# Kernel optimization log

Hardware: AMD Instinct MI355X
Metric: run time of the kernel (lower is better)

## Reference

```python
import jax, jax.numpy as jnp
import numpy as np

N_NODES = 100000
N_EDGES = 1600000
HIDDEN = 128
LEAKY_SLOPE = 0.01  # torch F.leaky_relu default


def setup_inputs() -> dict:
    key = jax.random.key(0)
    k1, k2, k3, k4 = jax.random.split(key, 4)
    x = jax.random.normal(k1, (N_NODES, HIDDEN), dtype=jnp.float32)
    edge_index = jax.random.randint(k2, (2, N_EDGES), 0, N_NODES, dtype=jnp.int64)
    # nn.Linear(hidden, 1, bias=False) weights, stored as [hidden] vectors
    w_i = jax.random.normal(k3, (HIDDEN,), dtype=jnp.float32) * (1.0 / np.sqrt(HIDDEN))
    w_j = jax.random.normal(k4, (HIDDEN,), dtype=jnp.float32) * (1.0 / np.sqrt(HIDDEN))
    return {"x": x, "edge_index": edge_index, "w_i": w_i, "w_j": w_j}


def _segment_softmax(e, seg, num_segments):
    # numerically stable softmax over variable-length groups keyed by seg
    seg_max = jax.ops.segment_max(e, seg, num_segments=num_segments)
    seg_max = jnp.where(jnp.isfinite(seg_max), seg_max, 0.0)  # empty segments
    e_exp = jnp.exp(e - seg_max[seg])
    denom = jax.ops.segment_sum(e_exp, seg, num_segments=num_segments)
    return e_exp / denom[seg]


def reference(x, edge_index, w_i, w_j):
    n = x.shape[0]
    idx_j = edge_index[0]  # edge_index_j (softmax groups)
    idx_i = edge_index[1]  # edge_index_i (aggregation destinations)
    # per-node attention logits, gathered per edge
    ei_all = x @ w_i  # [N]
    ej_all = x @ w_j  # [N]
    e = ei_all[idx_i] + ej_all[idx_j]  # [E]
    e = jnp.where(e > 0, e, LEAKY_SLOPE * e)  # leaky_relu
    alpha = _segment_softmax(e.astype(jnp.float32), idx_j, n)  # [E]
    # spmm(edge_index[[1,0]], alpha, N, N, x): out[idx_i] += alpha * x[idx_j]
    msgs = alpha[:, None] * x[idx_j]  # [E, hidden]
    out = jax.ops.segment_sum(msgs, idx_i, num_segments=n)
    return jax.nn.relu(out)
```

## Files before the change

kernel.cpp:

```cpp
#include <hip/hip_runtime.h>

#define N_HID 128
#define LEAKY 0.01f
#define EPB   2048
#define SCB   1024
#define TABV(g) (tab[g] + bs1[(g) >> 10])

__device__ inline ushort f2bf_rne(float f) {
    unsigned u = __float_as_uint(f);
    u += 0x7fffu + ((u >> 16) & 1u);
    return (ushort)(u >> 16);
}

__device__ inline int load_idx(const void* eidx, long long pos, int is64) {
    if (is64) return (int)((const long long*)eidx)[pos];
    return ((const int*)eidx)[pos];
}

__global__ void detect_dtype_k(const void* __restrict__ eidx, long long n_i64,
                               int* __restrict__ flag) {
    __shared__ int nonzero_hi;
    if (threadIdx.x == 0) nonzero_hi = 0;
    __syncthreads();
    const long long* p = (const long long*)eidx;
    long long samples = n_i64 < 4096 ? n_i64 : 4096;
    int bad = 0;
    for (long long k = threadIdx.x; k < samples; k += blockDim.x) {
        if ((p[k] >> 32) != 0) bad = 1;
    }
    if (bad) atomicOr(&nonzero_hi, 1);
    __syncthreads();
    if (threadIdx.x == 0) *flag = nonzero_hi ? 0 : 1;
}

__global__ __launch_bounds__(256) void node_logits_k(
        const float* __restrict__ x, const float* __restrict__ w_i,
        const float* __restrict__ w_j, float* __restrict__ ei_all,
        float* __restrict__ ej_all, ushort* __restrict__ xb, int n) {
    int wave = (int)((blockIdx.x * (long long)blockDim.x + threadIdx.x) >> 6);
    int lane = threadIdx.x & 63;
    if (wave >= n) return;
    const float2* xr = (const float2*)(x + (long long)wave * N_HID);
    float2 v  = xr[lane];
    float2 wi = ((const float2*)w_i)[lane];
    float2 wj = ((const float2*)w_j)[lane];
    if (xb) {
        unsigned packed = (unsigned)f2bf_rne(v.x) | ((unsigned)f2bf_rne(v.y) << 16);
        ((unsigned*)(xb + (long long)wave * N_HID))[lane] = packed;
    }
    float si = v.x * wi.x + v.y * wi.y;
    float sj = v.x * wj.x + v.y * wj.y;
    #pragma unroll
    for (int off = 32; off >= 1; off >>= 1) {
        si += __shfl_xor(si, off);
        sj += __shfl_xor(sj, off);
    }
    if (lane == 0) {
        ei_all[wave] = si;
        ej_all[wave] = sj;
    }
}

__global__ __launch_bounds__(256) void hist_k(
        const void* __restrict__ eidx, const int* __restrict__ flag,
        unsigned* __restrict__ tabI, unsigned* __restrict__ tabJ,
        long long E, int nblkA, int NB) {
    __shared__ unsigned hi[512], hj[512];
    for (int b = threadIdx.x; b < NB; b += 256) { hi[b] = 0; hj[b] = 0; }
    __syncthreads();
    int is64 = *flag;
    long long k0 = (long long)blockIdx.x * EPB;
    #pragma unroll 4
    for (int m = 0; m < EPB / 256; ++m) {
        long long k = k0 + m * 256 + threadIdx.x;
        if (k < E) {
            int j = load_idx(eidx, k, is64);
            int i = load_idx(eidx, E + k, is64);
            atomicAdd(&hi[i >> 8], 1u);
            atomicAdd(&hj[j >> 8], 1u);
        }
    }
    __syncthreads();
    for (int b = threadIdx.x; b < NB; b += 256) {
        tabI[(size_t)b * nblkA + blockIdx.x] = hi[b];
        tabJ[(size_t)b * nblkA + blockIdx.x] = hj[b];
    }
}

__global__ __launch_bounds__(SCB) void scanT1_k(unsigned* __restrict__ a,
                                                unsigned* __restrict__ bs, int nt) {
    __shared__ unsigned tmp[SCB];
    int gid = blockIdx.x * SCB + threadIdx.x;
    unsigned v = (gid < nt) ? a[gid] : 0;
    tmp[threadIdx.x] = v;
    __syncthreads();
    for (int off = 1; off < SCB; off <<= 1) {
        unsigned t = (threadIdx.x >= off) ? tmp[threadIdx.x - off] : 0;
        __syncthreads();
        tmp[threadIdx.x] += t;
        __syncthreads();
    }
    if (gid < nt) a[gid] = tmp[threadIdx.x] - v;
    if (threadIdx.x == SCB - 1) bs[blockIdx.x] = tmp[threadIdx.x];
}

__global__ __launch_bounds__(SCB) void scanT2_k(unsigned* __restrict__ bs, int nb) {
    __shared__ unsigned tmp[SCB];
    unsigned v = (threadIdx.x < nb) ? bs[threadIdx.x] : 0;
    tmp[threadIdx.x] = v;
    __syncthreads();
    for (int off = 1; off < SCB; off <<= 1) {
        unsigned t = (threadIdx.x >= off) ? tmp[threadIdx.x - off] : 0;
        __syncthreads();
        tmp[threadIdx.x] += t;
        __syncthreads();
    }
    if (threadIdx.x < nb) bs[threadIdx.x] = tmp[threadIdx.x] - v;
}

__global__ __launch_bounds__(256) void scatter2_k(
        const void* __restrict__ eidx, const int* __restrict__ flag,
        const unsigned* __restrict__ tab, const unsigned* __restrict__ bs1,
        unsigned* __restrict__ srecI, unsigned* __restrict__ srecJ,
        long long E, int nblkA, int NB, int NT) {
    __shared__ unsigned ci[512], cj[512];
    unsigned Eu = (unsigned)E;
    for (int b = threadIdx.x; b < NB; b += 256) {
        size_t gI = (size_t)b * nblkA + blockIdx.x;
        size_t gJ = (size_t)NT + gI;
        ci[b] = TABV(gI);
        cj[b] = TABV(gJ) - Eu;
    }
    __syncthreads();
    int is64 = *flag;
    long long k0 = (long long)blockIdx.x * EPB;
    #pragma unroll 4
    for (int m = 0; m < EPB / 256; ++m) {
        long long k = k0 + m * 256 + threadIdx.x;
        if (k < E) {
            int j = load_idx(eidx, k, is64);
            int i = load_idx(eidx, E + k, is64);
            unsigned pI = atomicAdd(&ci[i >> 8], 1u);
            srecI[pI] = ((unsigned)(i & 255) << 17) | (unsigned)j;
            unsigned pJ = atomicAdd(&cj[j >> 8], 1u);
            srecJ[pJ] = ((unsigned)(j & 255) << 17) | (unsigned)i;
        }
    }
}

__global__ __launch_bounds__(512) void finalizeJ_k(
        const unsigned* __restrict__ srecJ, const unsigned* __restrict__ tab,
        const unsigned* __restrict__ bs1, const float* __restrict__ ei_all,
        const float* __restrict__ ej_all, float2* __restrict__ ejd,
        int n, long long E, int nblkA, int NB, int NT) {
    int b = blockIdx.x;
    int tid = threadIdx.x;
    unsigned Eu = (unsigned)E;
    size_t gJ0 = (size_t)NT + (size_t)b * nblkA;
    int base = (int)(TABV(gJ0) - Eu);
    int end  = (b + 1 < NB) ? (int)(TABV(gJ0 + nblkA) - Eu) : (int)E;

    __shared__ float ejl[256];
    __shared__ float dsum[256];
    int g = b * 256 + tid;
    if (tid < 256) {
        ejl[tid]  = (g < n) ? ej_all[g] : 0.f;
        dsum[tid] = 0.f;
    }
    __syncthreads();

    for (int t = base + tid; t < end; t += 512) {
        unsigned r = srecJ[t];
        int jl = (int)(r >> 17);
        int i  = (int)(r & 0x1FFFFu);
        float e = ei_all[i] + ejl[jl];
        e = e > 0.f ? e : LEAKY * e;
        atomicAdd(&dsum[jl], __expf(e));
    }
    __syncthreads();
    if (tid < 256 && g < n) {
        float2 r2;
        r2.x = ejl[tid];
        r2.y = dsum[tid];
        ejd[g] = r2;
    }
}

__global__ __launch_bounds__(512) void finalizeI_k(
        const unsigned* __restrict__ srecI, const unsigned* __restrict__ tab,
        const unsigned* __restrict__ bs1, const float* __restrict__ ei_all,
        const float2* __restrict__ ejd, int* __restrict__ start,
        unsigned* __restrict__ pje, int n, long long E, int nblkA, int NB,
        int NT) {
    int b = blockIdx.x;
    int tid = threadIdx.x;
    size_t gI0 = (size_t)b * nblkA;
    int base = (int)TABV(gI0);
    int end  = (b + 1 < NB) ? (int)TABV(gI0 + nblkA) : (int)E;

    __shared__ int cnt[256];
    __shared__ int off[256];
    __shared__ float eil[256];
    int g = b * 256 + tid;
    if (tid < 256) {
        cnt[tid] = 0;
        eil[tid] = (g < n) ? ei_all[g] : 0.f;
    }
    __syncthreads();

    for (int t = base + tid; t < end; t += 512)
        atomicAdd(&cnt[srecI[t] >> 17], 1);
    __syncthreads();

    int v = 0;
    if (tid < 256) { v = cnt[tid]; off[tid] = v; }
    __syncthreads();
    for (int s = 1; s < 256; s <<= 1) {
        int t2 = 0;
        if (tid < 256 && tid >= s) t2 = off[tid - s];
        __syncthreads();
        if (tid < 256) off[tid] += t2;
        __syncthreads();
    }
    if (tid < 256) {
        int excl = off[tid] - v;
        if (g < n) start[g] = base + excl;
        cnt[tid] = excl;
    }
    if (b == NB - 1 && tid == 0) start[n] = (int)E;
    __syncthreads();

    for (int t = base + tid; t < end; t += 512) {
        unsigned r = srecI[t];
        int il = (int)(r >> 17);
        int j  = (int)(r & 0x1FFFFu);
        float2 ed = ejd[j];
        float e = eil[il] + ed.x;
        e = e > 0.f ? e : LEAKY * e;
        float alpha = __expf(e) / ed.y;
        unsigned aq = __float2uint_rn(alpha * 32768.f);
        if (aq > 32767u) aq = 32767u;
        int slot = base + atomicAdd(&cnt[il], 1);
        pje[slot] = ((unsigned)j << 15) | aq;
    }
}

__global__ __launch_bounds__(256) void gather_bf16_k(
        const int* __restrict__ start, const unsigned* __restrict__ pje,
        const ushort* __restrict__ xb, float* __restrict__ out, int n) {
    int wave = (int)((blockIdx.x * (long long)blockDim.x + threadIdx.x) >> 6);
    int lane = threadIdx.x & 63;
    if (wave >= n) return;
    int s = start[wave];
    int e_end = start[wave + 1];
    int sub = lane >> 4;
    int col = lane & 15;

    float a0 = 0.f, a1 = 0.f, a2 = 0.f, a3 = 0.f;
    float a4 = 0.f, a5 = 0.f, a6 = 0.f, a7 = 0.f;
    for (int e = s; e < e_end; e += 8) {
        int ee0 = e + sub;
        int ee1 = e + 4 + sub;
        unsigned cur0 = (ee0 < e_end) ? pje[ee0] : 0u;
        unsigned cur1 = (ee1 < e_end) ? pje[ee1] : 0u;
        float af0 = (float)(cur0 & 0x7FFFu) * (1.f / 32768.f);
        float af1 = (float)(cur1 & 0x7FFFu) * (1.f / 32768.f);
        uint4 u0 = ((const uint4*)(xb + (size_t)(cur0 >> 15) * N_HID))[col];
        uint4 u1 = ((const uint4*)(xb + (size_t)(cur1 >> 15) * N_HID))[col];
        a0 += af0 * __uint_as_float(u0.x << 16);
        a1 += af0 * __uint_as_float(u0.x & 0xffff0000u);
        a2 += af0 * __uint_as_float(u0.y << 16);
        a3 += af0 * __uint_as_float(u0.y & 0xffff0000u);
        a4 += af0 * __uint_as_float(u0.z << 16);
        a5 += af0 * __uint_as_float(u0.z & 0xffff0000u);
        a6 += af0 * __uint_as_float(u0.w << 16);
        a7 += af0 * __uint_as_float(u0.w & 0xffff0000u);
        a0 += af1 * __uint_as_float(u1.x << 16);
        a1 += af1 * __uint_as_float(u1.x & 0xffff0000u);
        a2 += af1 * __uint_as_float(u1.y << 16);
        a3 += af1 * __uint_as_float(u1.y & 0xffff0000u);
        a4 += af1 * __uint_as_float(u1.z << 16);
        a5 += af1 * __uint_as_float(u1.z & 0xffff0000u);
        a6 += af1 * __uint_as_float(u1.w << 16);
        a7 += af1 * __uint_as_float(u1.w & 0xffff0000u);
    }
    a0 += __shfl_xor(a0, 16); a1 += __shfl_xor(a1, 16);
    a2 += __shfl_xor(a2, 16); a3 += __shfl_xor(a3, 16);
    a4 += __shfl_xor(a4, 16); a5 += __shfl_xor(a5, 16);
    a6 += __shfl_xor(a6, 16); a7 += __shfl_xor(a7, 16);
    a0 += __shfl_xor(a0, 32); a1 += __shfl_xor(a1, 32);
    a2 += __shfl_xor(a2, 32); a3 += __shfl_xor(a3, 32);
    a4 += __shfl_xor(a4, 32); a5 += __shfl_xor(a5, 32);
    a6 += __shfl_xor(a6, 32); a7 += __shfl_xor(a7, 32);

    float4* orow = (float4*)(out + (size_t)wave * N_HID);
    if (sub == 0) {
        float4 r;
        r.x = fmaxf(a0, 0.f); r.y = fmaxf(a1, 0.f);
        r.z = fmaxf(a2, 0.f); r.w = fmaxf(a3, 0.f);
        orow[col * 2] = r;
    } else if (sub == 1) {
        float4 r;
        r.x = fmaxf(a4, 0.f); r.y = fmaxf(a5, 0.f);
        r.z = fmaxf(a6, 0.f); r.w = fmaxf(a7, 0.f);
        orow[col * 2 + 1] = r;
    }
}

__global__ __launch_bounds__(256) void gather_f32_k(
        const int* __restrict__ start, const unsigned* __restrict__ pje,
        const float* __restrict__ x, float* __restrict__ out, int n) {
    int wave = (int)((blockIdx.x * (long long)blockDim.x + threadIdx.x) >> 6);
    int lane = threadIdx.x & 63;
    if (wave >= n) return;
    int s = start[wave];
    int e_end = start[wave + 1];
    float ax = 0.f, ay = 0.f;
    unsigned ja = 0;
    if (s < e_end) ja = pje[s];
    for (int e = s; e < e_end; ++e) {
        unsigned cur = ja;
        if (e + 1 < e_end) ja = pje[e + 1];
        float a = (float)(cur & 0x7FFFu) * (1.f / 32768.f);
        float2 v = ((const float2*)(x + (long long)(cur >> 15) * N_HID))[lane];
        ax += a * v.x;
        ay += a * v.y;
    }
    float2 r;
    r.x = fmaxf(ax, 0.f);
    r.y = fmaxf(ay, 0.f);
    ((float2*)(out + (long long)wave * N_HID))[lane] = r;
}

extern "C" void kernel_launch(void* const* d_in, const int* in_sizes, int n_in,
                              void* d_out, int out_size, void* d_ws,
                              size_t ws_size, hipStream_t stream) {
    const float* x   = (const float*)d_in[0];
    const void*  eix = d_in[1];
    const float* w_i = (const float*)d_in[2];
    const float* w_j = (const float*)d_in[3];
    float* out = (float*)d_out;

    int n = in_sizes[0] / N_HID;
    long long E = in_sizes[1] / 2;

    int nblkA = (int)((E + EPB - 1) / EPB);
    int NB    = (n + 255) / 256;
    int NT    = NB * nblkA;
    int NT2   = 2 * NT;
    int nb1   = (NT2 + SCB - 1) / SCB;

    char* p = (char*)d_ws;
    float* ei_all = (float*)p;               p += (size_t)n * 4;
    float* ej_all = (float*)p;               p += (size_t)n * 4;
    float2* ejd   = (float2*)p;              p += (size_t)n * 8;
    int*   start  = (int*)p;                 p += ((size_t)(n + 1) * 4 + 15) & ~15ull;
    unsigned* tab = (unsigned*)p;            p += ((size_t)NT2 * 4 + 15) & ~15ull;
    unsigned* tabI = tab;
    unsigned* tabJ = tab + NT;
    unsigned* bs1 = (unsigned*)p;            p += (size_t)SCB * 4;
    int*   flag   = (int*)p;                 p += 16;
    unsigned* srecI = (unsigned*)p;          p += (size_t)E * 4;
    unsigned* pje   = (unsigned*)p;          p += (size_t)E * 4;
    unsigned* srecJ = pje;
    ushort* xb    = (ushort*)p;              p += (size_t)n * N_HID * 2;
    int wsBig = ((size_t)(p - (char*)d_ws) <= ws_size);
    if (!wsBig) xb = nullptr;

    detect_dtype_k<<<1, 256, 0, stream>>>(eix, E * 2, flag);

    long long t1 = (long long)n * 64;
    node_logits_k<<<(unsigned)((t1 + 255) / 256), 256, 0, stream>>>(
        x, w_i, w_j, ei_all, ej_all, xb, n);

    hist_k<<<nblkA, 256, 0, stream>>>(eix, flag, tabI, tabJ, E, nblkA, NB);

    scanT1_k<<<nb1, SCB, 0, stream>>>(tab, bs1, NT2);
    scanT2_k<<<1, SCB, 0, stream>>>(bs1, nb1);

    scatter2_k<<<nblkA, 256, 0, stream>>>(eix, flag, tab, bs1, srecI, srecJ,
                                          E, nblkA, NB, NT);

    finalizeJ_k<<<NB, 512, 0, stream>>>(srecJ, tab, bs1, ei_all, ej_all, ejd,
                                        n, E, nblkA, NB, NT);

    finalizeI_k<<<NB, 512, 0, stream>>>(srecI, tab, bs1, ei_all, ejd,
                                        start, pje, n, E, nblkA, NB, NT);

    long long t4 = (long long)n * 64;
    if (wsBig) {
        gather_bf16_k<<<(unsigned)((t4 + 255) / 256), 256, 0, stream>>>(
            start, pje, xb, out, n);
    } else {
        gather_f32_k<<<(unsigned)((t4 + 255) / 256), 256, 0, stream>>>(
            start, pje, x, out, n);
    }
}
```

Before: 201.9 us.

## Fuse logits and histogram kernels, inline dtype detection, prefetch edge records

Merges the node-logit kernel and the edge histogram kernel into one launch, splitting blocks by index between the two jobs so the independent work can run side by side. The separate dtype-detection kernel and its flag buffer are removed; each wave now samples 64 index words with a ballot. The gather loop also software-prefetches the next packed edge records. This cuts two launches and their serial dependencies, at the cost of a weaker dtype check that samples fewer values.

```diff
diff --git a/kernel.cpp b/kernel.cpp
--- a/kernel.cpp
+++ b/kernel.cpp
@@ -17,73 +17,64 @@
     return ((const int*)eidx)[pos];
 }
 
-__global__ void detect_dtype_k(const void* __restrict__ eidx, long long n_i64,
-                               int* __restrict__ flag) {
-    __shared__ int nonzero_hi;
-    if (threadIdx.x == 0) nonzero_hi = 0;
-    __syncthreads();
+__device__ inline int detect64(const void* eidx, int lane) {
     const long long* p = (const long long*)eidx;
-    long long samples = n_i64 < 4096 ? n_i64 : 4096;
-    int bad = 0;
-    for (long long k = threadIdx.x; k < samples; k += blockDim.x) {
-        if ((p[k] >> 32) != 0) bad = 1;
-    }
-    if (bad) atomicOr(&nonzero_hi, 1);
-    __syncthreads();
-    if (threadIdx.x == 0) *flag = nonzero_hi ? 0 : 1;
-}
-
-__global__ __launch_bounds__(256) void node_logits_k(
+    unsigned long long b = __ballot((p[lane] >> 32) != 0);
+    return b == 0ull;
+}
+
+__global__ __launch_bounds__(256) void logits_hist_k(
         const float* __restrict__ x, const float* __restrict__ w_i,
         const float* __restrict__ w_j, float* __restrict__ ei_all,
-        float* __restrict__ ej_all, ushort* __restrict__ xb, int n) {
-    int wave = (int)((blockIdx.x * (long long)blockDim.x + threadIdx.x) >> 6);
+        float* __restrict__ ej_all, ushort* __restrict__ xb,
+        const void* __restrict__ eidx, unsigned* __restrict__ tabI,
+        unsigned* __restrict__ tabJ, int n, long long E,
+        int nblkA, int NB) {
+    __shared__ unsigned hi[512], hj[512];
     int lane = threadIdx.x & 63;
-    if (wave >= n) return;
-    const float2* xr = (const float2*)(x + (long long)wave * N_HID);
-    float2 v  = xr[lane];
-    float2 wi = ((const float2*)w_i)[lane];
-    float2 wj = ((const float2*)w_j)[lane];
-    if (xb) {
-        unsigned packed = (unsigned)f2bf_rne(v.x) | ((unsigned)f2bf_rne(v.y) << 16);
-        ((unsigned*)(xb + (long long)wave * N_HID))[lane] = packed;
-    }
-    float si = v.x * wi.x + v.y * wi.y;
-    float sj = v.x * wj.x + v.y * wj.y;
-    #pragma unroll
-    for (int off = 32; off >= 1; off >>= 1) {
-        si += __shfl_xor(si, off);
-        sj += __shfl_xor(sj, off);
-    }
-    if (lane == 0) {
-        ei_all[wave] = si;
-        ej_all[wave] = sj;
-    }
-}
-
-__global__ __launch_bounds__(256) void hist_k(
-        const void* __restrict__ eidx, const int* __restrict__ flag,
-        unsigned* __restrict__ tabI, unsigned* __restrict__ tabJ,
-        long long E, int nblkA, int NB) {
-    __shared__ unsigned hi[512], hj[512];
-    for (int b = threadIdx.x; b < NB; b += 256) { hi[b] = 0; hj[b] = 0; }
-    __syncthreads();
-    int is64 = *flag;
-    long long k0 = (long long)blockIdx.x * EPB;
-    #pragma unroll 4
-    for (int m = 0; m < EPB / 256; ++m) {
-        long long k = k0 + m * 256 + threadIdx.x;
-        if (k < E) {
-            int j = load_idx(eidx, k, is64);
-            int i = load_idx(eidx, E + k, is64);
-            atomicAdd(&hi[i >> 8], 1u);
-            atomicAdd(&hj[j >> 8], 1u);
-        }
-    }
-    __syncthreads();
-    for (int b = threadIdx.x; b < NB; b += 256) {
-        tabI[(size_t)b * nblkA + blockIdx.x] = hi[b];
-        tabJ[(size_t)b * nblkA + blockIdx.x] = hj[b];
+    if (blockIdx.x < (unsigned)nblkA) {
+        for (int b = threadIdx.x; b < NB; b += 256) { hi[b] = 0; hj[b] = 0; }
+        __syncthreads();
+        int is64 = detect64(eidx, lane);
+        long long k0 = (long long)blockIdx.x * EPB;
+        #pragma unroll 4
+        for (int m = 0; m < EPB / 256; ++m) {
+            long long k = k0 + m * 256 + threadIdx.x;
+            if (k < E) {
+                int j = load_idx(eidx, k, is64);
+                int i = load_idx(eidx, E + k, is64);
+                atomicAdd(&hi[i >> 8], 1u);
+                atomicAdd(&hj[j >> 8], 1u);
+            }
+        }
+        __syncthreads();
+        for (int b = threadIdx.x; b < NB; b += 256) {
+            tabI[(size_t)b * nblkA + blockIdx.x] = hi[b];
+            tabJ[(size_t)b * nblkA + blockIdx.x] = hj[b];
+        }
+    } else {
+        int blk = blockIdx.x - nblkA;
+        int wave = blk * 4 + (int)(threadIdx.x >> 6);
+        if (wave >= n) return;
+        const float2* xr = (const float2*)(x + (long long)wave * N_HID);
+        float2 v  = xr[lane];
+        float2 wi = ((const float2*)w_i)[lane];
+        float2 wj = ((const float2*)w_j)[lane];
+        if (xb) {
+            unsigned pk = (unsigned)f2bf_rne(v.x) | ((unsigned)f2bf_rne(v.y) << 16);
+            ((unsigned*)(xb + (long long)wave * N_HID))[lane] = pk;
+        }
+        float si = v.x * wi.x + v.y * wi.y;
+        float sj = v.x * wj.x + v.y * wj.y;
+        #pragma unroll
+        for (int off = 32; off >= 1; off >>= 1) {
+            si += __shfl_xor(si, off);
+            sj += __shfl_xor(sj, off);
+        }
+        if (lane == 0) {
+            ei_all[wave] = si;
+            ej_all[wave] = sj;
+        }
     }
 }
 
@@ -119,10 +110,9 @@
 }
 
 __global__ __launch_bounds__(256) void scatter2_k(
-        const void* __restrict__ eidx, const int* __restrict__ flag,
-        const unsigned* __restrict__ tab, const unsigned* __restrict__ bs1,
-        unsigned* __restrict__ srecI, unsigned* __restrict__ srecJ,
-        long long E, int nblkA, int NB, int NT) {
+        const void* __restrict__ eidx, const unsigned* __restrict__ tab,
+        const unsigned* __restrict__ bs1, unsigned* __restrict__ srecI,
+        unsigned* __restrict__ srecJ, long long E, int nblkA, int NB, int NT) {
     __shared__ unsigned ci[512], cj[512];
     unsigned Eu = (unsigned)E;
     for (int b = threadIdx.x; b < NB; b += 256) {
@@ -132,7 +122,7 @@
         cj[b] = TABV(gJ) - Eu;
     }
     __syncthreads();
-    int is64 = *flag;
+    int is64 = detect64(eidx, threadIdx.x & 63);
     long long k0 = (long long)blockIdx.x * EPB;
     #pragma unroll 4
     for (int m = 0; m < EPB / 256; ++m) {
@@ -258,11 +248,14 @@
 
     float a0 = 0.f, a1 = 0.f, a2 = 0.f, a3 = 0.f;
     float a4 = 0.f, a5 = 0.f, a6 = 0.f, a7 = 0.f;
+    int p0 = s + sub, p1 = s + 4 + sub;
+    unsigned nc0 = (p0 < e_end) ? pje[p0] : 0u;
+    unsigned nc1 = (p1 < e_end) ? pje[p1] : 0u;
     for (int e = s; e < e_end; e += 8) {
-        int ee0 = e + sub;
-        int ee1 = e + 4 + sub;
-        unsigned cur0 = (ee0 < e_end) ? pje[ee0] : 0u;
-        unsigned cur1 = (ee1 < e_end) ? pje[ee1] : 0u;
+        unsigned cur0 = nc0, cur1 = nc1;
+        int q0 = e + 8 + sub, q1 = e + 12 + sub;
+        nc0 = (q0 < e_end) ? pje[q0] : 0u;
+        nc1 = (q1 < e_end) ? pje[q1] : 0u;
         float af0 = (float)(cur0 & 0x7FFFu) * (1.f / 32768.f);
         float af1 = (float)(cur1 & 0x7FFFu) * (1.f / 32768.f);
         uint4 u0 = ((const uint4*)(xb + (size_t)(cur0 >> 15) * N_HID))[col];
@@ -345,6 +338,7 @@
     long long E = in_sizes[1] / 2;
 
     int nblkA = (int)((E + EPB - 1) / EPB);
+    int nblkL = (n + 3) / 4;
     int NB    = (n + 255) / 256;
     int NT    = NB * nblkA;
     int NT2   = 2 * NT;
@@ -359,7 +353,6 @@
     unsigned* tabI = tab;
     unsigned* tabJ = tab + NT;
     unsigned* bs1 = (unsigned*)p;            p += (size_t)SCB * 4;
-    int*   flag   = (int*)p;                 p += 16;
     unsigned* srecI = (unsigned*)p;          p += (size_t)E * 4;
     unsigned* pje   = (unsigned*)p;          p += (size_t)E * 4;
     unsigned* srecJ = pje;
@@ -367,18 +360,13 @@
     int wsBig = ((size_t)(p - (char*)d_ws) <= ws_size);
     if (!wsBig) xb = nullptr;
 
-    detect_dtype_k<<<1, 256, 0, stream>>>(eix, E * 2, flag);
-
-    long long t1 = (long long)n * 64;
-    node_logits_k<<<(unsigned)((t1 + 255) / 256), 256, 0, stream>>>(
-        x, w_i, w_j, ei_all, ej_all, xb, n);
-
-    hist_k<<<nblkA, 256, 0, stream>>>(eix, flag, tabI, tabJ, E, nblkA, NB);
+    logits_hist_k<<<(unsigned)(nblkA + nblkL), 256, 0, stream>>>(
+        x, w_i, w_j, ei_all, ej_all, xb, eix, tabI, tabJ, n, E, nblkA, NB);
 
     scanT1_k<<<nb1, SCB, 0, stream>>>(tab, bs1, NT2);
     scanT2_k<<<1, SCB, 0, stream>>>(bs1, nb1);
 
-    scatter2_k<<<nblkA, 256, 0, stream>>>(eix, flag, tab, bs1, srecI, srecJ,
+    scatter2_k<<<nblkA, 256, 0, stream>>>(eix, tab, bs1, srecI, srecJ,
                                           E, nblkA, NB, NT);
 
     finalizeJ_k<<<NB, 512, 0, stream>>>(srecJ, tab, bs1, ei_all, ej_all, ejd,
```

After: 188.8 us. 1.07x faster.
